# Performance work log

Measured on AMD Instinct MI355X. Metric: run time of the kernel, lower is better.

## Reference

```python
import jax, jax.numpy as jnp
import numpy as np
from jax import lax

EPS_A = 1e-4


def _frft_1d(x, a):
    """Chirp-z shear FrFT along last axis. x: complex (..., N), a: scalar."""
    a = jnp.clip(a, EPS_A, 2.0 - EPS_A)
    N = x.shape[-1]
    x = jnp.fft.ifftshift(x, axes=-1)
    pi = jnp.pi
    alpha = a * pi / 2.0
    tan_a2 = jnp.tan(a * pi / 4.0)
    sin_a = jnp.sin(alpha)
    # replicate torch.arange(-N//2, N//2) with python floor division
    n = jnp.arange((-N) // 2, N // 2, dtype=jnp.float32)
    c1 = jnp.exp(-1j * pi * n ** 2 * tan_a2 / N)
    c2 = jnp.exp(-1j * pi * n ** 2 / (N * sin_a))
    y = jnp.fft.ifft(jnp.fft.fft(x * c1, axis=-1) * c2, axis=-1)
    y = y * c1 / jnp.sqrt(jnp.abs(sin_a) + 1e-12)
    return jnp.fft.fftshift(y, axes=-1)


def frft2d(x, ax, ay):
    """Separable 2-D FrFT: last axis with ay, then axis -2 with ax (matches torch loop order)."""
    X = x.astype(jnp.complex64)
    X = _frft_1d(X, ay)                      # along axis -1
    X = jnp.swapaxes(X, -1, -2)
    X = _frft_1d(X, ax)                      # along original axis -2
    return jnp.swapaxes(X, -1, -2)


def _spec2kernel(spec, alpha, polar_w):
    Co, Ci, k1, k2 = spec.shape
    S = spec.reshape(Co * Ci, 1, k1, k2)     # (CoCi, 1, k1, k2)
    Y = frft2d(S, alpha, alpha)              # complex (CoCi, 1, k1, k2)
    # polar repr, reduce=False -> concat(|Y|, angle(Y)/pi) on channel dim
    K = jnp.concatenate([jnp.abs(Y), jnp.angle(Y) / jnp.pi], axis=1)  # (CoCi, 2, k1, k2)
    K = (K * polar_w).sum(axis=1)            # (CoCi, k1, k2)
    return K.reshape(Co, Ci, k1, k2)


def setup_inputs() -> dict:
    key = jax.random.key(0)
    k1, k2, k3 = jax.random.split(key, 3)
    x = jax.random.normal(k1, (16, 64, 224, 224), dtype=jnp.float32)
    spec = jax.random.normal(k2, (64, 64, 3, 3), dtype=jnp.float32) * 0.001
    alpha = jnp.float32(0.5)
    polar_w = jnp.array([1.0, 0.0], dtype=jnp.float32).reshape(1, 2, 1, 1)
    return {"x": x, "spec": spec, "alpha": alpha, "polar_w": polar_w}


def reference(x, spec, alpha, polar_w):
    w = _spec2kernel(spec, alpha, polar_w)   # (64, 64, 3, 3)
    kh, kw = w.shape[2], w.shape[3]
    out = lax.conv_general_dilated(
        x, w,
        window_strides=(1, 1),
        padding=[(kh // 2, kh // 2), (kw // 2, kw // 2)],
        dimension_numbers=("NCHW", "OIHW", "NCHW"),
    )
    return out
```

## Files before the change

### kernel.cpp

```cpp
#include <hip/hip_runtime.h>
#include <math.h>


#define PI_F 3.14159265358979323846f

typedef __attribute__((ext_vector_type(8))) short  short8v;
typedef __attribute__((ext_vector_type(4))) float  f32x4;
typedef __attribute__((ext_vector_type(8))) unsigned short ush8;

#define XP_ELEMS   (16u * 226u * 226u * 64u)
#define XP_BYTES   ((size_t)XP_ELEMS * 2)
#define WTB_BYTES  (64 * 576 * 2)

__device__ __forceinline__ unsigned short f2b(float f) {
    union { float f; unsigned u; } v; v.f = f;
    unsigned u = v.u;
    return (unsigned short)((u + 0x7FFFu + ((u >> 16) & 1u)) >> 16);
}

struct C2 { float re, im; };
__device__ __forceinline__ C2 cmul(C2 a, C2 b) {
    return { a.re * b.re - a.im * b.im, a.re * b.im + a.im * b.re };
}
__device__ __forceinline__ C2 cadd3(C2 a, C2 b, C2 c) {
    return { a.re + b.re + c.re, a.im + b.im + c.im };
}
__device__ __forceinline__ C2 cexpi(float ph) {
    float s, c; sincosf(ph, &s, &c); return { c, s };
}
struct FrftConsts { C2 c1[3], c2[3]; float rs; };

__device__ __forceinline__ void frft3(C2& a0, C2& a1, C2& a2, const FrftConsts& K) {
    C2 u0 = cmul(a1, K.c1[0]);
    C2 u1 = cmul(a2, K.c1[1]);
    C2 u2 = cmul(a0, K.c1[2]);
    const C2 w  = { -0.5f, -0.8660254037844386f };
    const C2 wc = { -0.5f,  0.8660254037844386f };
    C2 U0 = cadd3(u0, u1, u2);
    C2 U1 = cadd3(u0, cmul(u1, w),  cmul(u2, wc));
    C2 U2 = cadd3(u0, cmul(u1, wc), cmul(u2, w));
    C2 V0 = cmul(U0, K.c2[0]);
    C2 V1 = cmul(U1, K.c2[1]);
    C2 V2 = cmul(U2, K.c2[2]);
    C2 v0 = cadd3(V0, V1, V2);
    C2 v1 = cadd3(V0, cmul(V1, wc), cmul(V2, w));
    C2 v2 = cadd3(V0, cmul(V1, w),  cmul(V2, wc));
    float s = K.rs * (1.0f / 3.0f);
    C2 y0 = cmul(v0, K.c1[0]); y0.re *= s; y0.im *= s;
    C2 y1 = cmul(v1, K.c1[1]); y1.re *= s; y1.im *= s;
    C2 y2 = cmul(v2, K.c1[2]); y2.re *= s; y2.im *= s;
    a0 = y2; a1 = y0; a2 = y1;
}

__global__ void spec2kernel(const float* __restrict__ spec,
                            const float* __restrict__ alpha_p,
                            const float* __restrict__ polar_w,
                            float* __restrict__ wt_f32,
                            unsigned short* __restrict__ wt_b16) {
    int f = blockIdx.x * blockDim.x + threadIdx.x;
    if (f >= 64 * 64) return;
    int co = f >> 6, ci = f & 63;

    float a = alpha_p[0];
    a = fminf(fmaxf(a, 1e-4f), 2.0f - 1e-4f);
    float alph  = a * (PI_F * 0.5f);
    float tana2 = tanf(a * (PI_F * 0.25f));
    float sina  = sinf(alph);

    FrftConsts K;
    const float n2[3] = { 4.0f, 1.0f, 0.0f };
#pragma unroll
    for (int k = 0; k < 3; ++k) {
        K.c1[k] = cexpi(-PI_F * n2[k] * tana2 * (1.0f / 3.0f));
        K.c2[k] = cexpi(-PI_F * n2[k] / (3.0f * sina));
    }
    K.rs = 1.0f / sqrtf(fabsf(sina) + 1e-12f);

    C2 z[3][3];
    const float* sp = spec + (size_t)f * 9;
#pragma unroll
    for (int r = 0; r < 3; ++r)
#pragma unroll
        for (int c = 0; c < 3; ++c)
            z[r][c] = { sp[r * 3 + c], 0.0f };

#pragma unroll
    for (int r = 0; r < 3; ++r) frft3(z[r][0], z[r][1], z[r][2], K);
#pragma unroll
    for (int c = 0; c < 3; ++c) frft3(z[0][c], z[1][c], z[2][c], K);

    float pw0 = polar_w[0], pw1 = polar_w[1];
#pragma unroll
    for (int r = 0; r < 3; ++r) {
#pragma unroll
        for (int c = 0; c < 3; ++c) {
            C2 y = z[r][c];
            float mag = sqrtf(y.re * y.re + y.im * y.im);
            float ang = atan2f(y.im, y.re) * (1.0f / PI_F);
            float wv = pw0 * mag + pw1 * ang;
            int tap = r * 3 + c;
            if (wt_f32) wt_f32[((size_t)ci * 9 + tap) * 64 + co] = wv;
            if (wt_b16) wt_b16[(size_t)co * 576 + tap * 64 + ci] = f2b(wv);
        }
    }
}

__global__ void transpose_x(const float* __restrict__ x,
                            unsigned short* __restrict__ xp) {
    __shared__ unsigned short lt[32][72];
    const int t  = threadIdx.x;
    const int w0 = blockIdx.x * 32;
    const int h  = blockIdx.y;
    const int n  = blockIdx.z;

#pragma unroll
    for (int i = 0; i < 2; ++i) {
        int task = t + i * 256;
        int ci = task >> 3, q = task & 7;
        float4 v = *reinterpret_cast<const float4*>(
            x + (((size_t)n * 64 + ci) * 224 + h) * 224 + w0 + 4 * q);
        lt[4 * q + 0][ci] = f2b(v.x);
        lt[4 * q + 1][ci] = f2b(v.y);
        lt[4 * q + 2][ci] = f2b(v.z);
        lt[4 * q + 3][ci] = f2b(v.w);
    }
    __syncthreads();
    int w = t >> 3, c = t & 7;
    ush8 v = *reinterpret_cast<const ush8*>(&lt[w][c * 8]);
    *reinterpret_cast<ush8*>(
        xp + ((size_t)(n * 226 + h + 1) * 226 + (w0 + w + 1)) * 64 + c * 8) = v;
}

__global__ void border_zero(unsigned short* __restrict__ xp) {
    int idx = blockIdx.x * 256 + threadIdx.x;
    if (idx >= 16 * 900 * 8) return;
    int c = idx & 7;
    int r = idx >> 3;
    int p = r % 900;
    int n = r / 900;
    int hh, ww;
    if (p < 226)      { hh = 0;   ww = p; }
    else if (p < 452) { hh = 225; ww = p - 226; }
    else {
        int p2 = p - 452;
        hh = 1 + (p2 >> 1);
        ww = (p2 & 1) ? 225 : 0;
    }
    ush8 z = {0, 0, 0, 0, 0, 0, 0, 0};
    *reinterpret_cast<ush8*>(
        xp + ((size_t)(n * 226 + hh) * 226 + ww) * 64 + c * 8) = z;
}

#define XS_BYTES 39168
#define WA_STRIDE 272
#define WB_STRIDE 336
#define WL_BYTES  21504

__global__ __launch_bounds__(256, 2) void conv_mfma(
        const unsigned short* __restrict__ xp,
        const unsigned short* __restrict__ wtb,
        float* __restrict__ out) {
    __shared__ __attribute__((aligned(128))) char lds[XS_BYTES + WL_BYTES];
    char* xs = lds;
    char* wl = lds + XS_BYTES;

    const int t    = threadIdx.x;
    const int lane = t & 63;
    const int wv   = t >> 6;
    const int li   = lane & 15;
    const int ch   = lane >> 4;
    const int wb   = blockIdx.x * 32;
    const int hb   = blockIdx.y * 16;
    const int n    = blockIdx.z;

    f32x4 acc[4][8];
#pragma unroll
    for (int i = 0; i < 4; ++i)
#pragma unroll
        for (int j = 0; j < 8; ++j) acc[i][j] = (f32x4){0.f, 0.f, 0.f, 0.f};

    const int sbase = 4 * wv * 34 + li;

    for (int half = 0; half < 2; ++half) {
        __syncthreads();
        for (int task = t; task < 2448; task += 256) {
            int c = task & 3, s = task >> 2;
            int row = s / 34, wsl = s - row * 34;
            ush8 v = *reinterpret_cast<const ush8*>(
                xp + ((size_t)(n * 226 + hb + row) * 226 + wb + wsl) * 64
                   + half * 32 + c * 8);
            int b = (s << 6) + (c << 4);
            b ^= ((s >> 1) & 3) << 4;
            *reinterpret_cast<ush8*>(xs + b) = v;
        }
        for (int task = t; task < 1024; task += 256) {
            int c = task & 3, r = task >> 2;
            int co = r >> 2, tapl = r & 3;
            ush8 v = *reinterpret_cast<const ush8*>(
                wtb + (size_t)co * 576 + tapl * 64 + half * 32 + c * 8);
            *reinterpret_cast<ush8*>(wl + co * WA_STRIDE + tapl * 64 + (c << 4)) = v;
        }
        __syncthreads();

#pragma unroll
        for (int tap = 0; tap < 4; ++tap) {
            const int r_off = tap / 3, c_off = tap % 3;
            short8v af[4], bf[8];
#pragma unroll
            for (int cs = 0; cs < 4; ++cs) {
                int b = (cs * 16 + li) * WA_STRIDE + tap * 64 + (ch << 4);
                af[cs] = *reinterpret_cast<const short8v*>(wl + b);
            }
#pragma unroll
            for (int p = 0; p < 8; ++p) {
                int s = sbase + ((p >> 1) + r_off) * 34 + (p & 1) * 16 + c_off;
                int b = (s << 6) + (ch << 4);
                b ^= ((s >> 1) & 3) << 4;
                bf[p] = *reinterpret_cast<const short8v*>(xs + b);
            }
#pragma unroll
            for (int cs = 0; cs < 4; ++cs)
#pragma unroll
                for (int p = 0; p < 8; ++p)
                    acc[cs][p] = __builtin_amdgcn_mfma_f32_16x16x32_bf16(
                        af[cs], bf[p], acc[cs][p], 0, 0, 0);
        }

        __syncthreads();
        for (int task = t; task < 1280; task += 256) {
            int c = task & 3, r = task >> 2;
            int co = r / 5, tapl = r - co * 5;
            ush8 v = *reinterpret_cast<const ush8*>(
                wtb + (size_t)co * 576 + (4 + tapl) * 64 + half * 32 + c * 8);
            *reinterpret_cast<ush8*>(wl + co * WB_STRIDE + tapl * 64 + (c << 4)) = v;
        }
        __syncthreads();

#pragma unroll
        for (int tap = 4; tap < 9; ++tap) {
            const int r_off = tap / 3, c_off = tap % 3;
            short8v af[4], bf[8];
#pragma unroll
            for (int cs = 0; cs < 4; ++cs) {
                int b = (cs * 16 + li) * WB_STRIDE + (tap - 4) * 64 + (ch << 4);
                af[cs] = *reinterpret_cast<const short8v*>(wl + b);
            }
#pragma unroll
            for (int p = 0; p < 8; ++p) {
                int s = sbase + ((p >> 1) + r_off) * 34 + (p & 1) * 16 + c_off;
                int b = (s << 6) + (ch << 4);
                b ^= ((s >> 1) & 3) << 4;
                bf[p] = *reinterpret_cast<const short8v*>(xs + b);
            }
#pragma unroll
            for (int cs = 0; cs < 4; ++cs)
#pragma unroll
                for (int p = 0; p < 8; ++p)
                    acc[cs][p] = __builtin_amdgcn_mfma_f32_16x16x32_bf16(
                        af[cs], bf[p], acc[cs][p], 0, 0, 0);
        }
    }

#pragma unroll
    for (int cs = 0; cs < 4; ++cs) {
#pragma unroll
        for (int p = 0; p < 8; ++p) {
            int h = hb + wv * 4 + (p >> 1);
            int w = wb + (p & 1) * 16 + li;
#pragma unroll
            for (int j = 0; j < 4; ++j) {
                int co = cs * 16 + ch * 4 + j;
                out[((size_t)(n * 64 + co) * 224 + h) * 224 + w] = acc[cs][p][j];
            }
        }
    }
}

#define WTILE 112
__global__ __launch_bounds__(256) void conv3x3(const float* __restrict__ x,
                                               const float* __restrict__ wt,
                                               float* __restrict__ out) {
    __shared__ float xsm[4][3][114];
    __shared__ float wsh[4][9][64];

    const int wtile = blockIdx.x;
    const int h     = blockIdx.y;
    const int n     = blockIdx.z;
    const int wb    = wtile * WTILE;
    const int t     = threadIdx.x;
    const int co    = t & 63;
    const int g     = t >> 6;
    const int base  = g * 28;

    float acc[28];
#pragma unroll
    for (int p = 0; p < 28; ++p) acc[p] = 0.0f;

    for (int cb = 0; cb < 16; ++cb) {
        __syncthreads();
        for (int e = t; e < 4 * 3 * 114; e += 256) {
            int ci_l = e / 342;
            int rem  = e - ci_l * 342;
            int r    = rem / 114;
            int px   = rem - r * 114;
            int gy   = h + r - 1;
            int gx   = wb + px - 1;
            float v  = 0.0f;
            if ((unsigned)gy < 224u && (unsigned)gx < 224u)
                v = x[(((size_t)n * 64 + cb * 4 + ci_l) * 224 + gy) * 224 + gx];
            xsm[ci_l][r][px] = v;
        }
        for (int e = t; e < 4 * 9 * 64; e += 256) {
            int ci_l = e / 576;
            int rem  = e - ci_l * 576;
            wsh[ci_l][rem / 64][rem & 63] = wt[((size_t)(cb * 4 + ci_l)) * 576 + rem];
        }
        __syncthreads();

#pragma unroll
        for (int ci_l = 0; ci_l < 4; ++ci_l) {
            float w0[3], w1[3], w2[3];
#pragma unroll
            for (int r = 0; r < 3; ++r) {
                w0[r] = wsh[ci_l][r * 3 + 0][co];
                w1[r] = wsh[ci_l][r * 3 + 1][co];
                w2[r] = wsh[ci_l][r * 3 + 2][co];
            }
#pragma unroll
            for (int r = 0; r < 3; ++r) {
                float x0 = xsm[ci_l][r][base + 0];
                float x1 = xsm[ci_l][r][base + 1];
#pragma unroll
                for (int p = 0; p < 28; ++p) {
                    float x2 = xsm[ci_l][r][base + p + 2];
                    acc[p] += w0[r] * x0 + w1[r] * x1 + w2[r] * x2;
                    x0 = x1; x1 = x2;
                }
            }
        }
    }

    float* op = out + (((size_t)n * 64 + co) * 224 + h) * 224 + wb + base;
#pragma unroll
    for (int p = 0; p < 28; p += 4) {
        float4 v = { acc[p], acc[p + 1], acc[p + 2], acc[p + 3] };
        *reinterpret_cast<float4*>(op + p) = v;
    }
}

extern "C" void kernel_launch(void* const* d_in, const int* in_sizes, int n_in,
                              void* d_out, int out_size, void* d_ws, size_t ws_size,
                              hipStream_t stream) {
    const float* x     = (const float*)d_in[0];
    const float* spec  = (const float*)d_in[1];
    const float* alpha = (const float*)d_in[2];
    const float* pw    = (const float*)d_in[3];
    float* out = (float*)d_out;

    if (ws_size >= XP_BYTES + WTB_BYTES) {
        unsigned short* xp  = (unsigned short*)d_ws;
        unsigned short* wtb = (unsigned short*)((char*)d_ws + XP_BYTES);

        spec2kernel<<<16, 256, 0, stream>>>(spec, alpha, pw, nullptr, wtb);
        transpose_x<<<dim3(7, 224, 16), 256, 0, stream>>>(x, xp);
        border_zero<<<450, 256, 0, stream>>>(xp);
        conv_mfma<<<dim3(7, 14, 16), 256, 0, stream>>>(xp, wtb, out);
    } else {
        float* wt = (float*)d_ws;
        spec2kernel<<<16, 256, 0, stream>>>(spec, alpha, pw, wt, nullptr);
        conv3x3<<<dim3(2, 224, 16), 256, 0, stream>>>(x, wt, out);
    }
}
```

Before: 514.4 us.

## Stage full weights and both channel halves in LDS once, single-pass conv

```diff
diff --git a/kernel.cpp b/kernel.cpp
--- a/kernel.cpp
+++ b/kernel.cpp
@@ -100,7 +100,8 @@
             float wv = pw0 * mag + pw1 * ang;
             int tap = r * 3 + c;
             if (wt_f32) wt_f32[((size_t)ci * 9 + tap) * 64 + co] = wv;
-            if (wt_b16) wt_b16[(size_t)co * 576 + tap * 64 + ci] = f2b(wv);
+            if (wt_b16) wt_b16[(size_t)co * 576 + (ci >> 5) * 288 + tap * 32
+                               + (ci & 31)] = f2b(wv);
         }
     }
 }
@@ -110,25 +111,28 @@
     __shared__ unsigned short lt[32][72];
     const int t  = threadIdx.x;
     const int w0 = blockIdx.x * 32;
-    const int h  = blockIdx.y;
     const int n  = blockIdx.z;
 
-#pragma unroll
-    for (int i = 0; i < 2; ++i) {
-        int task = t + i * 256;
-        int ci = task >> 3, q = task & 7;
-        float4 v = *reinterpret_cast<const float4*>(
-            x + (((size_t)n * 64 + ci) * 224 + h) * 224 + w0 + 4 * q);
-        lt[4 * q + 0][ci] = f2b(v.x);
-        lt[4 * q + 1][ci] = f2b(v.y);
-        lt[4 * q + 2][ci] = f2b(v.z);
-        lt[4 * q + 3][ci] = f2b(v.w);
-    }
-    __syncthreads();
-    int w = t >> 3, c = t & 7;
-    ush8 v = *reinterpret_cast<const ush8*>(&lt[w][c * 8]);
-    *reinterpret_cast<ush8*>(
-        xp + ((size_t)(n * 226 + h + 1) * 226 + (w0 + w + 1)) * 64 + c * 8) = v;
+    for (int it = 0; it < 4; ++it) {
+        const int h = blockIdx.y * 4 + it;
+        if (it) __syncthreads();
+#pragma unroll
+        for (int i = 0; i < 2; ++i) {
+            int task = t + i * 256;
+            int ci = task >> 3, q = task & 7;
+            float4 v = *reinterpret_cast<const float4*>(
+                x + (((size_t)n * 64 + ci) * 224 + h) * 224 + w0 + 4 * q);
+            lt[4 * q + 0][ci] = f2b(v.x);
+            lt[4 * q + 1][ci] = f2b(v.y);
+            lt[4 * q + 2][ci] = f2b(v.z);
+            lt[4 * q + 3][ci] = f2b(v.w);
+        }
+        __syncthreads();
+        int w = t >> 3, c = t & 7;
+        ush8 v = *reinterpret_cast<const ush8*>(&lt[w][c * 8]);
+        *reinterpret_cast<ush8*>(
+            xp + ((size_t)(n * 226 + h + 1) * 226 + (w0 + w + 1)) * 64 + c * 8) = v;
+    }
 }
 
 __global__ void border_zero(unsigned short* __restrict__ xp) {
@@ -151,114 +155,85 @@
         xp + ((size_t)(n * 226 + hh) * 226 + ww) * 64 + c * 8) = z;
 }
 
-#define XS_BYTES 39168
-#define WA_STRIDE 272
-#define WB_STRIDE 336
-#define WL_BYTES  21504
-
-__global__ __launch_bounds__(256, 2) void conv_mfma(
+#define WCO_STRIDE  1168
+#define WLDS_BYTES  (64 * WCO_STRIDE)
+#define XHALF_BYTES 39168
+#define LDS_TOTAL   (WLDS_BYTES + 2 * XHALF_BYTES)
+
+__global__ __launch_bounds__(256, 1) void conv_mfma(
         const unsigned short* __restrict__ xp,
         const unsigned short* __restrict__ wtb,
         float* __restrict__ out) {
-    __shared__ __attribute__((aligned(128))) char lds[XS_BYTES + WL_BYTES];
-    char* xs = lds;
-    char* wl = lds + XS_BYTES;
+    __shared__ __attribute__((aligned(128))) char lds[LDS_TOTAL];
+    char* wl = lds;
+    char* xs = lds + WLDS_BYTES;
 
     const int t    = threadIdx.x;
     const int lane = t & 63;
-    const int wv   = t >> 6;
     const int li   = lane & 15;
     const int ch   = lane >> 4;
+    const int wv   = t >> 6;
     const int wb   = blockIdx.x * 32;
     const int hb   = blockIdx.y * 16;
     const int n    = blockIdx.z;
 
-    f32x4 acc[4][8];
-#pragma unroll
-    for (int i = 0; i < 4; ++i)
-#pragma unroll
-        for (int j = 0; j < 8; ++j) acc[i][j] = (f32x4){0.f, 0.f, 0.f, 0.f};
-
-    const int sbase = 4 * wv * 34 + li;
-
-    for (int half = 0; half < 2; ++half) {
-        __syncthreads();
-        for (int task = t; task < 2448; task += 256) {
-            int c = task & 3, s = task >> 2;
-            int row = s / 34, wsl = s - row * 34;
+#pragma unroll
+    for (int i = 0; i < 18; ++i) {
+        int c2 = t + i * 256;
+        int co = c2 / 72, r = c2 - co * 72;
+        int kk = r >> 2, c4 = r & 3;
+        ush8 v = *reinterpret_cast<const ush8*>(
+            wtb + (size_t)co * 576 + kk * 32 + c4 * 8);
+        *reinterpret_cast<ush8*>(wl + co * WCO_STRIDE + kk * 64 + (c4 << 4)) = v;
+    }
+#pragma unroll
+    for (int i = 0; i < 20; ++i) {
+        int task = t + i * 256;
+        if (task < 4896) {
+            int half = task >= 2448 ? 1 : 0;
+            int r    = task - half * 2448;
+            int s    = r >> 2, c = r & 3;
+            int row  = s / 34, wsl = s - row * 34;
             ush8 v = *reinterpret_cast<const ush8*>(
                 xp + ((size_t)(n * 226 + hb + row) * 226 + wb + wsl) * 64
                    + half * 32 + c * 8);
-            int b = (s << 6) + (c << 4);
-            b ^= ((s >> 1) & 3) << 4;
-            *reinterpret_cast<ush8*>(xs + b) = v;
-        }
-        for (int task = t; task < 1024; task += 256) {
-            int c = task & 3, r = task >> 2;
-            int co = r >> 2, tapl = r & 3;
-            ush8 v = *reinterpret_cast<const ush8*>(
-                wtb + (size_t)co * 576 + tapl * 64 + half * 32 + c * 8);
-            *reinterpret_cast<ush8*>(wl + co * WA_STRIDE + tapl * 64 + (c << 4)) = v;
-        }
-        __syncthreads();
-
-#pragma unroll
-        for (int tap = 0; tap < 4; ++tap) {
-            const int r_off = tap / 3, c_off = tap % 3;
-            short8v af[4], bf[8];
-#pragma unroll
-            for (int cs = 0; cs < 4; ++cs) {
-                int b = (cs * 16 + li) * WA_STRIDE + tap * 64 + (ch << 4);
-                af[cs] = *reinterpret_cast<const short8v*>(wl + b);
-            }
-#pragma unroll
-            for (int p = 0; p < 8; ++p) {
-                int s = sbase + ((p >> 1) + r_off) * 34 + (p & 1) * 16 + c_off;
-                int b = (s << 6) + (ch << 4);
-                b ^= ((s >> 1) & 3) << 4;
-                bf[p] = *reinterpret_cast<const short8v*>(xs + b);
-            }
-#pragma unroll
-            for (int cs = 0; cs < 4; ++cs)
-#pragma unroll
-                for (int p = 0; p < 8; ++p)
-                    acc[cs][p] = __builtin_amdgcn_mfma_f32_16x16x32_bf16(
-                        af[cs], bf[p], acc[cs][p], 0, 0, 0);
-        }
-
-        __syncthreads();
-        for (int task = t; task < 1280; task += 256) {
-            int c = task & 3, r = task >> 2;
-            int co = r / 5, tapl = r - co * 5;
-            ush8 v = *reinterpret_cast<const ush8*>(
-                wtb + (size_t)co * 576 + (4 + tapl) * 64 + half * 32 + c * 8);
-            *reinterpret_cast<ush8*>(wl + co * WB_STRIDE + tapl * 64 + (c << 4)) = v;
-        }
-        __syncthreads();
-
-#pragma unroll
-        for (int tap = 4; tap < 9; ++tap) {
-            const int r_off = tap / 3, c_off = tap % 3;
-            short8v af[4], bf[8];
-#pragma unroll
-            for (int cs = 0; cs < 4; ++cs) {
-                int b = (cs * 16 + li) * WB_STRIDE + (tap - 4) * 64 + (ch << 4);
-                af[cs] = *reinterpret_cast<const short8v*>(wl + b);
-            }
-#pragma unroll
-            for (int p = 0; p < 8; ++p) {
-                int s = sbase + ((p >> 1) + r_off) * 34 + (p & 1) * 16 + c_off;
-                int b = (s << 6) + (ch << 4);
-                b ^= ((s >> 1) & 3) << 4;
-                bf[p] = *reinterpret_cast<const short8v*>(xs + b);
-            }
-#pragma unroll
-            for (int cs = 0; cs < 4; ++cs)
-#pragma unroll
-                for (int p = 0; p < 8; ++p)
-                    acc[cs][p] = __builtin_amdgcn_mfma_f32_16x16x32_bf16(
-                        af[cs], bf[p], acc[cs][p], 0, 0, 0);
-        }
+            int b = (s << 6) + ((c ^ ((s >> 1) & 3)) << 4);
+            *reinterpret_cast<ush8*>(xs + half * XHALF_BYTES + b) = v;
+        }
+    }
+    __syncthreads();
+
+    f32x4 acc[4][8];
+#pragma unroll
+    for (int i = 0; i < 4; ++i)
+#pragma unroll
+        for (int j = 0; j < 8; ++j) acc[i][j] = (f32x4){0.f, 0.f, 0.f, 0.f};
+
+    const int sbase = 4 * wv * 34 + li;
+
+#pragma unroll
+    for (int kk = 0; kk < 18; ++kk) {
+        const int half  = kk / 9;
+        const int tap   = kk - half * 9;
+        const int r_off = tap / 3, c_off = tap % 3;
+        short8v af[4], bf[8];
+#pragma unroll
+        for (int cs = 0; cs < 4; ++cs) {
+            af[cs] = *reinterpret_cast<const short8v*>(
+                wl + (cs * 16 + li) * WCO_STRIDE + kk * 64 + (ch << 4));
+        }
+#pragma unroll
+        for (int p = 0; p < 8; ++p) {
+            int s = sbase + ((p >> 1) + r_off) * 34 + (p & 1) * 16 + c_off;
+            int b = (s << 6) + ((ch ^ ((s >> 1) & 3)) << 4);
+            bf[p] = *reinterpret_cast<const short8v*>(xs + half * XHALF_BYTES + b);
+        }
+#pragma unroll
+        for (int cs = 0; cs < 4; ++cs)
+#pragma unroll
+            for (int p = 0; p < 8; ++p)
+                acc[cs][p] = __builtin_amdgcn_mfma_f32_16x16x32_bf16(
+                    af[cs], bf[p], acc[cs][p], 0, 0, 0);
     }
 
 #pragma unroll
@@ -361,13 +336,13 @@
         unsigned short* xp  = (unsigned short*)d_ws;
         unsigned short* wtb = (unsigned short*)((char*)d_ws + XP_BYTES);
 
-        spec2kernel<<<16, 256, 0, stream>>>(spec, alpha, pw, nullptr, wtb);
-        transpose_x<<<dim3(7, 224, 16), 256, 0, stream>>>(x, xp);
+        spec2kernel<<<64, 64, 0, stream>>>(spec, alpha, pw, nullptr, wtb);
+        transpose_x<<<dim3(7, 56, 16), 256, 0, stream>>>(x, xp);
         border_zero<<<450, 256, 0, stream>>>(xp);
         conv_mfma<<<dim3(7, 14, 16), 256, 0, stream>>>(xp, wtb, out);
     } else {
         float* wt = (float*)d_ws;
-        spec2kernel<<<16, 256, 0, stream>>>(spec, alpha, pw, wt, nullptr);
+        spec2kernel<<<64, 64, 0, stream>>>(spec, alpha, pw, wt, nullptr);
         conv3x3<<<dim3(2, 224, 16), 256, 0, stream>>>(x, wt, out);
     }
 }
```

Result: faster. 438.4 us (-14.8%).
